# Performance work log

Hardware: AMD Instinct MI355X
Metric: run time of the kernel (lower is better)

Reference implementation:

```python
import jax, jax.numpy as jnp
import numpy as np

B, C, H, W, L = 8, 512, 32, 32, 10
CQK = C // 8
EPS = 1e-5


def conv1x1(x, Wt, b):
    # 1x1 conv == per-pixel linear: [O,C] x [B,C,H,W] -> [B,O,H,W]
    return jnp.einsum('oc,bchw->bohw', Wt, x) + b[None, :, None, None]


def batchnorm_train(x, g, b):
    # BatchNorm2d in training mode: batch stats over (N,H,W), biased variance
    m = x.mean(axis=(0, 2, 3))
    v = x.var(axis=(0, 2, 3))
    inv = jax.lax.rsqrt(v + EPS)
    return (x - m[None, :, None, None]) * (g * inv)[None, :, None, None] + b[None, :, None, None]


def setup_inputs() -> dict:
    key = jax.random.key(0)
    ks = jax.random.split(key, 24)
    s = lambda n: 1.0 / np.sqrt(n)
    inp = {
        'x': jax.random.normal(ks[0], (B, C, H, W), jnp.float32),
        'y': jax.random.normal(ks[1], (B, C, H, W), jnp.float32),
        'x_hidden': jax.random.normal(ks[2], (L, B, C, H, W), jnp.float32),
        'y_hidden': jax.random.normal(ks[3], (L, B, C, H, W), jnp.float32),
        'qW': jax.random.normal(ks[4], (CQK, C), jnp.float32) * s(C),
        'qb': jnp.zeros((CQK,), jnp.float32),
        'kW': jax.random.normal(ks[5], (CQK, C), jnp.float32) * s(C),
        'kb': jnp.zeros((CQK,), jnp.float32),
        'v1W': jax.random.normal(ks[6], (C, C), jnp.float32) * s(C),
        'v1b': jnp.zeros((C,), jnp.float32),
        'v2W': jax.random.normal(ks[7], (C, C), jnp.float32) * s(C),
        'v2b': jnp.zeros((C,), jnp.float32),
        'hw1': jnp.ones((L,), jnp.float32),
        'hw2': jnp.ones((L,), jnp.float32),
        'g1W1': jax.random.normal(ks[8], (64, C), jnp.float32) * s(C),
        'g1b1': jnp.zeros((64,), jnp.float32),
        'g1W2': jax.random.normal(ks[9], (1, 64), jnp.float32) * s(64),
        'g1b2': jnp.zeros((1,), jnp.float32),
        'g2W1': jax.random.normal(ks[10], (64, C), jnp.float32) * s(C),
        'g2b1': jnp.zeros((64,), jnp.float32),
        'g2W2': jax.random.normal(ks[11], (1, 64), jnp.float32) * s(64),
        'g2b2': jnp.zeros((1,), jnp.float32),
        'rW1': jax.random.normal(ks[12], (C, C), jnp.float32) * s(C),
        'rb1': jnp.zeros((C,), jnp.float32),
        'bn1g': jnp.ones((C,), jnp.float32),
        'bn1b': jnp.zeros((C,), jnp.float32),
        'rW2': jax.random.normal(ks[13], (C, C), jnp.float32) * s(C),
        'rb2': jnp.zeros((C,), jnp.float32),
        'bn2g': jnp.ones((C,), jnp.float32),
        'bn2b': jnp.zeros((C,), jnp.float32),
    }
    return inp


def reference(x, y, x_hidden, y_hidden, qW, qb, kW, kb, v1W, v1b, v2W, v2b,
              hw1, hw2, g1W1, g1b1, g1W2, g1b2, g2W1, g2b1, g2W2, g2b2,
              rW1, rb1, bn1g, bn1b, rW2, rb2, bn2g, bn2b):
    b_, c_, h_, w_ = x.shape
    n = h_ * w_

    def residual(z):
        z1 = jax.nn.relu(batchnorm_train(conv1x1(z, rW1, rb1), bn1g, bn1b))
        return batchnorm_train(conv1x1(z1, rW2, rb2), bn2g, bn2b)

    # QKV projections (1x1 convs), flattened to tokens
    q = conv1x1(x, qW, qb).reshape(b_, CQK, n).transpose(0, 2, 1)   # [B,N,Cqk]
    k = conv1x1(y, kW, kb).reshape(b_, CQK, n)                       # [B,Cqk,N]
    v1 = conv1x1(x, v1W, v1b).reshape(b_, c_, n)                     # [B,C,N]
    v2 = conv1x1(y, v2W, v2b).reshape(b_, c_, n)

    attn = jax.nn.softmax(jnp.einsum('bnd,bdm->bnm', q, k), axis=-1)  # [B,N,N]
    out1 = jnp.einsum('bcn,bmn->bcm', v1, attn).reshape(b_, c_, h_, w_)  # v1 @ attn^T
    out2 = jnp.einsum('bcn,bnm->bcm', v2, attn).reshape(b_, c_, h_, w_)  # v2 @ attn

    # hidden-layer weighted channel means -> gamma scalars
    num_layers = min(x_hidden.shape[0], L)
    xw = jax.nn.softmax(hw1[:num_layers])
    yw = jax.nn.softmax(hw2[:num_layers])
    x_hw = jnp.einsum('l,lbc->bc', xw, x_hidden[:num_layers].mean(axis=(3, 4)))  # [B,C]
    y_hw = jnp.einsum('l,lbc->bc', yw, y_hidden[:num_layers].mean(axis=(3, 4)))

    def gamma_gen(v, W1, b1, W2, b2):
        h1 = jax.nn.relu(v @ W1.T + b1)
        return (h1 @ W2.T + b2).reshape(b_, 1, 1, 1)

    gamma1 = gamma_gen(x_hw, g1W1, g1b1, g1W2, g1b2)
    gamma2 = gamma_gen(y_hw, g2W1, g2b1, g2W2, g2b2)

    out1 = jax.nn.relu(residual(gamma1 * out1) + x)
    out2 = jax.nn.relu(residual(gamma2 * out2) + y)
    return out1, out2
```

## Files before the change

kernel.cpp:

```cpp
#include <hip/hip_runtime.h>

#define BB 8
#define CC 512
#define NT 1024
#define LL 10
#define DQK 64
#define BN_EPS 1e-5f

using u16 = unsigned short;
typedef __attribute__((ext_vector_type(8))) short short8;
typedef __attribute__((ext_vector_type(4))) float f32x4;

__device__ __forceinline__ float waveSum(float v) {
#pragma unroll
  for (int o = 32; o; o >>= 1) v += __shfl_down(v, o, 64);
  return v;
}
__device__ __forceinline__ float waveMax(float v) {
#pragma unroll
  for (int o = 32; o; o >>= 1) v = fmaxf(v, __shfl_down(v, o, 64));
  return v;
}
__device__ __forceinline__ u16 f2bf(float f) {
  unsigned u = __float_as_uint(f);
  u += 0x7FFFu + ((u >> 16) & 1u);
  return (u16)(u >> 16);
}
__device__ __forceinline__ float bf2f(u16 h) {
  return __uint_as_float(((unsigned)h) << 16);
}
__device__ __forceinline__ void g2l16(const u16* g, void* l) {
  __builtin_amdgcn_global_load_lds(
      (const __attribute__((address_space(1))) unsigned int*)g,
      (__attribute__((address_space(3))) unsigned int*)l, 16, 0, 0);
}

__global__ __launch_bounds__(256) void hidden_mean_kernel(
    const float* __restrict__ xh, const float* __restrict__ yh, float* __restrict__ lm) {
  const int LBC = LL * BB * CC;
  int wid = blockIdx.x * 4 + (threadIdx.x >> 6);
  int lane = threadIdx.x & 63;
  int row0 = wid * 4;
  const float* src = xh;
  int r0 = row0;
  if (row0 >= LBC) { src = yh; r0 = row0 - LBC; }
  const float4* p = (const float4*)(src + (size_t)r0 * NT);
  float s[4];
#pragma unroll
  for (int r = 0; r < 4; r++) {
    float4 a = p[r * 256 + lane];
    float4 b = p[r * 256 + 64 + lane];
    float4 c = p[r * 256 + 128 + lane];
    float4 d = p[r * 256 + 192 + lane];
    s[r] = ((a.x + a.y) + (a.z + a.w)) + ((b.x + b.y) + (b.z + b.w)) +
           ((c.x + c.y) + (c.z + c.w)) + ((d.x + d.y) + (d.z + d.w));
  }
#pragma unroll
  for (int r = 0; r < 4; r++) s[r] = waveSum(s[r]);
  if (lane == 0) {
    float4 o = {s[0] * (1.0f / NT), s[1] * (1.0f / NT),
                s[2] * (1.0f / NT), s[3] * (1.0f / NT)};
    *(float4*)&lm[row0] = o;
  }
}

__global__ __launch_bounds__(256) void gamma_kernel(
    const float* __restrict__ lm,
    const float* __restrict__ hw1, const float* __restrict__ hw2,
    const float* __restrict__ g1W1, const float* __restrict__ g1b1,
    const float* __restrict__ g1W2, const float* __restrict__ g1b2,
    const float* __restrict__ g2W1, const float* __restrict__ g2b1,
    const float* __restrict__ g2W2, const float* __restrict__ g2b2,
    float* __restrict__ gamma) {
  int which = blockIdx.x >> 3;
  int b = blockIdx.x & 7;
  const float* hw = which ? hw2 : hw1;
  const float* W1 = which ? g2W1 : g1W1;
  const float* b1 = which ? g2b1 : g1b1;
  const float* W2 = which ? g2W2 : g1W2;
  const float* b2 = which ? g2b2 : g1b2;
  __shared__ float sxhw[CC];
  __shared__ float wsm[LL];
  if (threadIdx.x == 0) {
    float mx = -1e30f;
    for (int l = 0; l < LL; l++) mx = fmaxf(mx, hw[l]);
    float den = 0.f, e[LL];
    for (int l = 0; l < LL; l++) { e[l] = __expf(hw[l] - mx); den += e[l]; }
    for (int l = 0; l < LL; l++) wsm[l] = e[l] / den;
  }
  __syncthreads();
  const float* lmb = lm + (size_t)which * LL * BB * CC + b * CC;
  for (int c = threadIdx.x; c < CC; c += blockDim.x) {
    float a = 0.f;
    for (int l = 0; l < LL; l++) a += wsm[l] * lmb[l * BB * CC + c];
    sxhw[c] = a;
  }
  __syncthreads();
  float contrib = 0.f;
  if (threadIdx.x < 64) {
    int d = threadIdx.x;
    float a = b1[d];
    const float* wr = W1 + d * CC;
    for (int c = 0; c < CC; c++) a = fmaf(wr[c], sxhw[c], a);
    contrib = W2[d] * fmaxf(a, 0.f);
  }
  contrib = waveSum(contrib);
  if (threadIdx.x == 0) gamma[which * BB + b] = contrib + b2[0];
}

struct WcvtArgs {
  const float* src[4];
  int nblk[5];
};
__global__ __launch_bounds__(256) void wcvt_kernel(WcvtArgs a, u16* __restrict__ dst) {
  int blk = blockIdx.x;
  int seg = 0;
  while (blk >= a.nblk[seg + 1]) seg++;
  int rel = blk - a.nblk[seg];
  const float4* s4 = (const float4*)a.src[seg];
  float4 v = s4[(size_t)rel * 256 + threadIdx.x];
  uint2 o;
  o.x = (unsigned)f2bf(v.x) | ((unsigned)f2bf(v.y) << 16);
  o.y = (unsigned)f2bf(v.z) | ((unsigned)f2bf(v.w) << 16);
  ((uint2*)dst)[(size_t)blk * 256 + threadIdx.x] = o;
}

__global__ __launch_bounds__(256) void wcvt_split_kernel(
    const float* __restrict__ qW, const float* __restrict__ kW,
    u16* __restrict__ qh, u16* __restrict__ ql,
    u16* __restrict__ kh, u16* __restrict__ kl,
    const float* __restrict__ qb, const float* __restrict__ kb,
    const float* __restrict__ v1b, const float* __restrict__ v2b,
    float* __restrict__ qkb, float* __restrict__ vb) {
  int blk = blockIdx.x;
  if (blk == 0) {
    int t = threadIdx.x;
    if (t < 64) qkb[t] = qb[t];
    else if (t < 128) qkb[t] = kb[t - 64];
    vb[t] = v1b[t]; vb[t + 256] = v1b[t + 256];
    vb[t + 512] = v2b[t]; vb[t + 768] = v2b[t + 256];
  }
  const float* src = (blk < 32) ? qW : kW;
  u16* dh = (blk < 32) ? qh : kh;
  u16* dl = (blk < 32) ? ql : kl;
  int rel = blk & 31;
  float4 v = ((const float4*)src)[(size_t)rel * 256 + threadIdx.x];
  u16 h0 = f2bf(v.x), h1 = f2bf(v.y), h2 = f2bf(v.z), h3 = f2bf(v.w);
  u16 l0 = f2bf(v.x - bf2f(h0)), l1 = f2bf(v.y - bf2f(h1));
  u16 l2 = f2bf(v.z - bf2f(h2)), l3 = f2bf(v.w - bf2f(h3));
  uint2 oh, ol;
  oh.x = (unsigned)h0 | ((unsigned)h1 << 16); oh.y = (unsigned)h2 | ((unsigned)h3 << 16);
  ol.x = (unsigned)l0 | ((unsigned)l1 << 16); ol.y = (unsigned)l2 | ((unsigned)l3 << 16);
  ((uint2*)dh)[(size_t)rel * 256 + threadIdx.x] = oh;
  ((uint2*)dl)[(size_t)rel * 256 + threadIdx.x] = ol;
}

__global__ __launch_bounds__(256) void transpose_xy_kernel(
    const float* __restrict__ x, const float* __restrict__ y,
    u16* __restrict__ xth, u16* __restrict__ xtl,
    u16* __restrict__ yth, u16* __restrict__ ytl) {
  __shared__ float t[64][65];
  int z = blockIdx.z;
  const float* src = (z < 8) ? x : y;
  u16* dh = (z < 8) ? xth : yth;
  u16* dl = (z < 8) ? xtl : ytl;
  int b = z & 7;
  int n0 = blockIdx.x * 64, c0 = blockIdx.y * 64;
  int tc = threadIdx.x & 63, tr = threadIdx.x >> 6;
  const float* S = src + ((size_t)b * CC + c0) * NT + n0;
#pragma unroll
  for (int r = 0; r < 16; r++) {
    int c = tr + r * 4;
    t[c][tc] = S[(size_t)c * NT + tc];
  }
  __syncthreads();
  size_t base = ((size_t)b * NT + n0) * CC + c0;
#pragma unroll
  for (int r = 0; r < 16; r++) {
    int n = tr + r * 4;
    float v = t[tc][n];
    u16 h = f2bf(v);
    dh[base + (size_t)n * CC + tc] = h;
    dl[base + (size_t)n * CC + tc] = f2bf(v - bf2f(h));
  }
}

__global__ __launch_bounds__(256) void transpose_attn_kernel(
    const u16* __restrict__ attn, u16* __restrict__ attnT) {
  __shared__ u16 t[64][66];
  int b = blockIdx.z;
  int n0 = blockIdx.y * 64, m0 = blockIdx.x * 64;
  int tc = threadIdx.x & 63, tr = threadIdx.x >> 6;
  const u16* S = attn + ((size_t)b * NT + n0) * NT + m0;
#pragma unroll
  for (int r = 0; r < 16; r++) {
    int nr = tr + r * 4;
    t[nr][tc] = S[(size_t)nr * NT + tc];
  }
  __syncthreads();
  u16* D = attnT + ((size_t)b * NT + m0) * NT + n0;
#pragma unroll
  for (int r = 0; r < 16; r++) {
    int mr = tr + r * 4;
    D[(size_t)mr * NT + tc] = t[tc][mr];
  }
}

template <int BN>
__global__ __launch_bounds__(256) void gemm_bf16(
    const u16* __restrict__ A, long long sA, int lda,
    const u16* __restrict__ B, long long sB, long long sB2, int ldb,
    void* __restrict__ C, long long sC, int ldc,
    int K, int storef32,
    const float* __restrict__ bias_row, int brs,
    const float* __restrict__ scale) {
  constexpr int BM = 128, BK = 32;
  constexpr int WN = (BN == 128) ? 2 : 1;
  constexpr int WM = 4 / WN;
  constexpr int FM = BM / (WM * 16);
  constexpr int FN = BN / (WN * 16);
  __shared__ u16 As[BM * BK];
  __shared__ u16 Bs[BN * BK];
  const int bz = blockIdx.z;
  const int i0 = blockIdx.y * BM;
  const int j0 = blockIdx.x * BN;
  const u16* Ab = A + (size_t)bz * sA + (size_t)i0 * lda;
  const u16* Bb = B + (size_t)(bz & 7) * sB + (size_t)(bz >> 3) * sB2 + (size_t)j0 * ldb;
  const int tid = threadIdx.x;
  const int lane = tid & 63;
  const int wave = tid >> 6;
  const int wr = wave / WN, wc = wave % WN;
  const int fr = lane & 15;
  const int kg = lane >> 4;
  const int arow = tid >> 2;
  const int aq = tid & 3;

  f32x4 acc[FM][FN] = {};

  for (int k0 = 0; k0 < K; k0 += BK) {
#pragma unroll
    for (int c = 0; c < (BM * BK * 2) / 4096; c++)
      g2l16(Ab + (size_t)(arow + c * 64) * lda + k0 + aq * 8,
            (char*)As + c * 4096 + tid * 16);
#pragma unroll
    for (int c = 0; c < (BN * BK * 2) / 4096; c++)
      g2l16(Bb + (size_t)(arow + c * 64) * ldb + k0 + aq * 8,
            (char*)Bs + c * 4096 + tid * 16);
    __syncthreads();
    short8 fa[FM], fb[FN];
#pragma unroll
    for (int i = 0; i < FM; i++)
      fa[i] = *(const short8*)&As[(wr * FM * 16 + i * 16 + fr) * BK + kg * 8];
#pragma unroll
    for (int j = 0; j < FN; j++)
      fb[j] = *(const short8*)&Bs[(wc * FN * 16 + j * 16 + fr) * BK + kg * 8];
#pragma unroll
    for (int i = 0; i < FM; i++)
#pragma unroll
      for (int j = 0; j < FN; j++)
        acc[i][j] = __builtin_amdgcn_mfma_f32_16x16x32_bf16(fa[i], fb[j], acc[i][j], 0, 0, 0);
    __syncthreads();
  }

  const float scl = scale ? scale[bz] : 1.0f;
  const float* brow = bias_row ? bias_row + (size_t)bz * brs : nullptr;
  float* Cf = (float*)C + (size_t)bz * sC;
  u16* Ch = (u16*)C + (size_t)bz * sC;
#pragma unroll
  for (int i = 0; i < FM; i++) {
#pragma unroll
    for (int j = 0; j < FN; j++) {
      int col = j0 + wc * FN * 16 + j * 16 + fr;
#pragma unroll
      for (int r = 0; r < 4; r++) {
        int row = i0 + wr * FM * 16 + i * 16 + kg * 4 + r;
        float rb = brow ? brow[row] : 0.0f;
        float v = (acc[i][j][r] + rb) * scl;
        if (storef32) Cf[(size_t)row * ldc + col] = v;
        else Ch[(size_t)row * ldc + col] = f2bf(v);
      }
    }
  }
}

__global__ __launch_bounds__(256) void gemm_split(
    const u16* __restrict__ Ah_, const u16* __restrict__ Al_, long long sA, int lda,
    const u16* __restrict__ Bh_, const u16* __restrict__ Bl_, long long sB, int ldb,
    float* __restrict__ Cf, u16* __restrict__ Ch, u16* __restrict__ Cl,
    long long sC, int ldc, int K, const float* __restrict__ bias_col, int bcs) {
  constexpr int BM = 128, BN = 64, BK = 32;
  constexpr int FM = 2, FN = 4;
  __shared__ u16 Ahs[BM * BK];
  __shared__ u16 Als[BM * BK];
  __shared__ u16 Bhs[BN * BK];
  __shared__ u16 Bls[BN * BK];
  const int bz = blockIdx.z;
  const int i0 = blockIdx.y * BM;
  const int j0 = blockIdx.x * BN;
  const u16* Abh = Ah_ + (size_t)bz * sA + (size_t)i0 * lda;
  const u16* Abl = Al_ + (size_t)bz * sA + (size_t)i0 * lda;
  const u16* Bbh = Bh_ + (size_t)bz * sB + (size_t)j0 * ldb;
  const u16* Bbl = Bl_ + (size_t)bz * sB + (size_t)j0 * ldb;
  const int tid = threadIdx.x;
  const int lane = tid & 63;
  const int wr = tid >> 6;
  const int fr = lane & 15;
  const int kg = lane >> 4;
  const int arow = tid >> 2;
  const int aq = tid & 3;

  f32x4 acc[FM][FN] = {};

  for (int k0 = 0; k0 < K; k0 += BK) {
#pragma unroll
    for (int c = 0; c < 2; c++) {
      g2l16(Abh + (size_t)(arow + c * 64) * lda + k0 + aq * 8,
            (char*)Ahs + c * 4096 + tid * 16);
      g2l16(Abl + (size_t)(arow + c * 64) * lda + k0 + aq * 8,
            (char*)Als + c * 4096 + tid * 16);
    }
    g2l16(Bbh + (size_t)arow * ldb + k0 + aq * 8, (char*)Bhs + tid * 16);
    g2l16(Bbl + (size_t)arow * ldb + k0 + aq * 8, (char*)Bls + tid * 16);
    __syncthreads();
    short8 fah[FM], fal[FM], fbh[FN], fbl[FN];
#pragma unroll
    for (int i = 0; i < FM; i++) {
      fah[i] = *(const short8*)&Ahs[(wr * 32 + i * 16 + fr) * BK + kg * 8];
      fal[i] = *(const short8*)&Als[(wr * 32 + i * 16 + fr) * BK + kg * 8];
    }
#pragma unroll
    for (int j = 0; j < FN; j++) {
      fbh[j] = *(const short8*)&Bhs[(j * 16 + fr) * BK + kg * 8];
      fbl[j] = *(const short8*)&Bls[(j * 16 + fr) * BK + kg * 8];
    }
#pragma unroll
    for (int i = 0; i < FM; i++)
#pragma unroll
      for (int j = 0; j < FN; j++) {
        acc[i][j] = __builtin_amdgcn_mfma_f32_16x16x32_bf16(fah[i], fbh[j], acc[i][j], 0, 0, 0);
        acc[i][j] = __builtin_amdgcn_mfma_f32_16x16x32_bf16(fah[i], fbl[j], acc[i][j], 0, 0, 0);
        acc[i][j] = __builtin_amdgcn_mfma_f32_16x16x32_bf16(fal[i], fbh[j], acc[i][j], 0, 0, 0);
      }
    __syncthreads();
  }

  const float* bcol = bias_col ? bias_col + (size_t)bz * bcs : nullptr;
  float* Cfb = Cf ? Cf + (size_t)bz * sC : nullptr;
  u16* Chb = Ch ? Ch + (size_t)bz * sC : nullptr;
  u16* Clb = Cl ? Cl + (size_t)bz * sC : nullptr;
#pragma unroll
  for (int i = 0; i < FM; i++) {
#pragma unroll
    for (int j = 0; j < FN; j++) {
      int col = j0 + j * 16 + fr;
      float cb = bcol ? bcol[col] : 0.0f;
#pragma unroll
      for (int r = 0; r < 4; r++) {
        int row = i0 + wr * 32 + i * 16 + kg * 4 + r;
        float v = acc[i][j][r] + cb;
        if (Cfb) {
          Cfb[(size_t)row * ldc + col] = v;
        } else {
          u16 h = f2bf(v);
          Chb[(size_t)row * ldc + col] = h;
          Clb[(size_t)row * ldc + col] = f2bf(v - bf2f(h));
        }
      }
    }
  }
}

__global__ __launch_bounds__(256) void softmax_bf_kernel(
    const float* __restrict__ S, u16* __restrict__ A) {
  const float4* row = (const float4*)(S + (size_t)blockIdx.x * NT);
  float4 v = row[threadIdx.x];
  __shared__ float sb[4];
  __shared__ float broad;
  int lane = threadIdx.x & 63, wid = threadIdx.x >> 6;
  float mx = fmaxf(fmaxf(v.x, v.y), fmaxf(v.z, v.w));
  mx = waveMax(mx);
  if (lane == 0) sb[wid] = mx;
  __syncthreads();
  if (threadIdx.x == 0) broad = fmaxf(fmaxf(sb[0], sb[1]), fmaxf(sb[2], sb[3]));
  __syncthreads();
  mx = broad;
  v.x = __expf(v.x - mx); v.y = __expf(v.y - mx);
  v.z = __expf(v.z - mx); v.w = __expf(v.w - mx);
  float s = v.x + v.y + v.z + v.w;
  s = waveSum(s);
  __syncthreads();
  if (lane == 0) sb[wid] = s;
  __syncthreads();
  if (threadIdx.x == 0) broad = sb[0] + sb[1] + sb[2] + sb[3];
  __syncthreads();
  float inv = 1.0f / broad;
  uint2 o;
  o.x = (unsigned)f2bf(v.x * inv) | ((unsigned)f2bf(v.y * inv) << 16);
  o.y = (unsigned)f2bf(v.z * inv) | ((unsigned)f2bf(v.w * inv) << 16);
  ((uint2*)(A + (size_t)blockIdx.x * NT))[threadIdx.x] = o;
}

__global__ __launch_bounds__(256) void bnstats_tm_part(
    const u16* __restrict__ Z, float* __restrict__ pS, float* __restrict__ pS2) {
  int blk = blockIdx.x;
  int chain = blk >> 8, bl = blk & 255;
  int c2 = threadIdx.x;
  float s0 = 0, s1 = 0, q0 = 0, q1 = 0;
  const u16* base = Z + (size_t)blk * 32 * CC;
#pragma unroll 4
  for (int r = 0; r < 32; r++) {
    unsigned u = *(const unsigned*)(base + (size_t)r * CC + c2 * 2);
    float a = bf2f((u16)u), b = bf2f((u16)(u >> 16));
    s0 += a; q0 += a * a; s1 += b; q1 += b * b;
  }
  size_t co = (size_t)chain * 512;
  pS[(co + c2 * 2) * 256 + bl] = s0;
  pS[(co + c2 * 2 + 1) * 256 + bl] = s1;
  pS2[(co + c2 * 2) * 256 + bl] = q0;
  pS2[(co + c2 * 2 + 1) * 256 + bl] = q1;
}
__global__ __launch_bounds__(256) void bnstats_tm_reduce(
    const float* __restrict__ pS, const float* __restrict__ pS2,
    const float* __restrict__ g, const float* __restrict__ bet,
    float* __restrict__ scale, float* __restrict__ shift) {
  int cg = blockIdx.x;
  int c = cg & 511;
  float s = pS[(size_t)cg * 256 + threadIdx.x];
  float s2 = pS2[(size_t)cg * 256 + threadIdx.x];
  s = waveSum(s); s2 = waveSum(s2);
  __shared__ float sb[8];
  int lane = threadIdx.x & 63, wid = threadIdx.x >> 6;
  if (lane == 0) { sb[wid] = s; sb[wid + 4] = s2; }
  __syncthreads();
  if (threadIdx.x == 0) {
    float S = sb[0] + sb[1] + sb[2] + sb[3];
    float S2 = sb[4] + sb[5] + sb[6] + sb[7];
    const float invn = 1.0f / (BB * NT);
    float mean = S * invn;
    float var = S2 * invn - mean * mean;
    float inv = rsqrtf(var + BN_EPS);
    float sc = g[c] * inv;
    scale[cg] = sc;
    shift[cg] = bet[c] - mean * sc;
  }
}

__global__ __launch_bounds__(256) void bnstats_cm(
    const u16* __restrict__ Z, const float* __restrict__ g, const float* __restrict__ bet,
    float* __restrict__ scale, float* __restrict__ shift) {
  int cg = blockIdx.x;
  int c = cg & 511;
  const uint2* row = (const uint2*)(Z + (size_t)cg * (BB * NT));
  float s = 0, s2 = 0;
#pragma unroll
  for (int it = 0; it < 8; it++) {
    uint2 u = row[threadIdx.x + it * 256];
    float a = bf2f((u16)u.x), b = bf2f((u16)(u.x >> 16));
    float d = bf2f((u16)u.y), e = bf2f((u16)(u.y >> 16));
    s += a + b + d + e;
    s2 += a * a + b * b + d * d + e * e;
  }
  s = waveSum(s); s2 = waveSum(s2);
  __shared__ float sb[8];
  int lane = threadIdx.x & 63, wid = threadIdx.x >> 6;
  if (lane == 0) { sb[wid] = s; sb[wid + 4] = s2; }
  __syncthreads();
  if (threadIdx.x == 0) {
    float S = sb[0] + sb[1] + sb[2] + sb[3];
    float S2 = sb[4] + sb[5] + sb[6] + sb[7];
    const float invn = 1.0f / (BB * NT);
    float mean = S * invn;
    float var = S2 * invn - mean * mean;
    float inv = rsqrtf(var + BN_EPS);
    float sc = g[c] * inv;
    scale[cg] = sc;
    shift[cg] = bet[c] - mean * sc;
  }
}

__global__ __launch_bounds__(256) void bn_apply_kernel(
    const u16* __restrict__ Z, u16* __restrict__ Zo,
    const float* __restrict__ scale, const float* __restrict__ shift) {
  size_t e4 = (size_t)blockIdx.x * 256 + threadIdx.x;
  int chain = (int)(e4 >> 20);
  int c = (int)(e4 & 127) * 4 + chain * 512;
  uint2 u = ((const uint2*)Z)[e4];
  float a = bf2f((u16)u.x), b = bf2f((u16)(u.x >> 16));
  float d = bf2f((u16)u.y), e = bf2f((u16)(u.y >> 16));
  a = fmaxf(fmaf(a, scale[c], shift[c]), 0.f);
  b = fmaxf(fmaf(b, scale[c + 1], shift[c + 1]), 0.f);
  d = fmaxf(fmaf(d, scale[c + 2], shift[c + 2]), 0.f);
  e = fmaxf(fmaf(e, scale[c + 3], shift[c + 3]), 0.f);
  uint2 o;
  o.x = (unsigned)f2bf(a) | ((unsigned)f2bf(b) << 16);
  o.y = (unsigned)f2bf(d) | ((unsigned)f2bf(e) << 16);
  ((uint2*)Zo)[e4] = o;
}

__global__ __launch_bounds__(256) void bn_final_kernel(
    const u16* __restrict__ Z2, const float* __restrict__ X, const float* __restrict__ Y,
    const float* __restrict__ scale, const float* __restrict__ shift,
    float* __restrict__ Out) {
  size_t e = (size_t)blockIdx.x * 256 + threadIdx.x;
  int chain = (int)(e >> 20);
  size_t ec = e & 1048575;
  int c = (int)(ec >> 11);
  int r = (int)(ec & 2047);
  int b = r >> 8;
  uint2 u = ((const uint2*)Z2)[e];
  float a0 = bf2f((u16)u.x), a1 = bf2f((u16)(u.x >> 16));
  float a2 = bf2f((u16)u.y), a3 = bf2f((u16)(u.y >> 16));
  float sc = scale[c + chain * 512], sh = shift[c + chain * 512];
  size_t xi = ((size_t)b * CC + c) * 256 + (r & 255);
  const float* Xs = chain ? Y : X;
  float4 xv = ((const float4*)Xs)[xi];
  float4 o;
  o.x = fmaxf(fmaf(a0, sc, sh) + xv.x, 0.f);
  o.y = fmaxf(fmaf(a1, sc, sh) + xv.y, 0.f);
  o.z = fmaxf(fmaf(a2, sc, sh) + xv.z, 0.f);
  o.w = fmaxf(fmaf(a3, sc, sh) + xv.w, 0.f);
  ((float4*)(Out + (size_t)chain * 4194304))[xi] = o;
}

extern "C" void kernel_launch(void* const* d_in, const int* in_sizes, int n_in,
                              void* d_out, int out_size, void* d_ws, size_t ws_size,
                              hipStream_t stream) {
  (void)in_sizes; (void)n_in; (void)out_size; (void)ws_size;
  const float* x    = (const float*)d_in[0];
  const float* y    = (const float*)d_in[1];
  const float* xh   = (const float*)d_in[2];
  const float* yh   = (const float*)d_in[3];
  const float* qW   = (const float*)d_in[4];
  const float* qb   = (const float*)d_in[5];
  const float* kW   = (const float*)d_in[6];
  const float* kb   = (const float*)d_in[7];
  const float* v1W  = (const float*)d_in[8];
  const float* v1b  = (const float*)d_in[9];
  const float* v2W  = (const float*)d_in[10];
  const float* v2b  = (const float*)d_in[11];
  const float* hw1  = (const float*)d_in[12];
  const float* hw2  = (const float*)d_in[13];
  const float* g1W1 = (const float*)d_in[14];
  const float* g1b1 = (const float*)d_in[15];
  const float* g1W2 = (const float*)d_in[16];
  const float* g1b2 = (const float*)d_in[17];
  const float* g2W1 = (const float*)d_in[18];
  const float* g2b1 = (const float*)d_in[19];
  const float* g2W2 = (const float*)d_in[20];
  const float* g2b2 = (const float*)d_in[21];
  const float* rW1  = (const float*)d_in[22];
  const float* bn1g = (const float*)d_in[24];
  const float* bn1b = (const float*)d_in[25];
  const float* rW2  = (const float*)d_in[26];
  const float* bn2g = (const float*)d_in[28];
  const float* bn2b = (const float*)d_in[29];
  float* out = (float*)d_out;

  float* ws  = (float*)d_ws;
  float* lm  = ws;
  float* gam = ws + 81920;
  float* scA = ws + 81936;
  float* shA = ws + 82960;
  float* qkb = ws + 83984;
  float* vb  = ws + 84112;
  float* pS  = ws + 85136;
  float* pS2 = ws + 347280;
  float* S   = ws + 609424;
  u16* U     = (u16*)(ws + 8998032);
  u16* Wqh = U;
  u16* Wql = U + 32768;
  u16* Wkh = U + 65536;
  u16* Wkl = U + 98304;
  u16* Wv1 = U + 131072;
  u16* Wv2 = U + 393216;
  u16* Wr1 = U + 655360;
  u16* Wr2 = U + 917504;
  u16* xth = U + 1179648;
  u16* yth = xth + 4194304;
  u16* xtl = yth + 4194304;
  u16* ytl = xtl + 4194304;
  u16* q_h = ytl + 4194304;
  u16* q_l = q_h + 524288;
  u16* k_h = q_l + 524288;
  u16* k_l = k_h + 524288;
  u16* v1  = k_l + 524288;
  u16* v2  = v1 + 4194304;
  u16* attn  = v2 + 4194304;
  u16* attnT = attn + 8388608;
  u16* o1t = xth;
  u16* z0  = v1;
  u16* z1  = xth;
  u16* z2  = attn;

  WcvtArgs wa;
  wa.src[0] = v1W; wa.src[1] = v2W; wa.src[2] = rW1; wa.src[3] = rW2;
  int pref[5] = {0, 256, 512, 768, 1024};
  for (int i = 0; i < 5; i++) wa.nblk[i] = pref[i];
  wcvt_kernel<<<1024, 256, 0, stream>>>(wa, Wv1);
  wcvt_split_kernel<<<64, 256, 0, stream>>>(qW, kW, Wqh, Wql, Wkh, Wkl,
                                            qb, kb, v1b, v2b, qkb, vb);
  hidden_mean_kernel<<<5120, 256, 0, stream>>>(xh, yh, lm);
  gamma_kernel<<<16, 256, 0, stream>>>(lm, hw1, hw2, g1W1, g1b1, g1W2, g1b2,
                                       g2W1, g2b1, g2W2, g2b2, gam);

  transpose_xy_kernel<<<dim3(16, 8, 16), 256, 0, stream>>>(x, y, xth, xtl, yth, ytl);

  gemm_bf16<128><<<dim3(64, 4, 2), 256, 0, stream>>>(
      Wv1, 262144, CC, xth, 4194304, 0, CC, v1, 4194304, BB * NT, CC, 0, vb, 512, nullptr);
  gemm_split<<<dim3(1, 64, 2), 256, 0, stream>>>(
      xth, xtl, 4194304, CC, Wqh, Wql, 65536, CC,
      nullptr, q_h, q_l, 1048576, DQK, CC, qkb, 64);

  gemm_split<<<dim3(16, 8, 8), 256, 0, stream>>>(
      q_h, q_l, (long long)NT * DQK, DQK, k_h, k_l, (long long)NT * DQK, DQK,
      S, nullptr, nullptr, (long long)NT * NT, NT, DQK, nullptr, 0);
  softmax_bf_kernel<<<BB * NT, 256, 0, stream>>>(S, attn);
  transpose_attn_kernel<<<dim3(16, 16, 8), 256, 0, stream>>>(attn, attnT);

  gemm_bf16<128><<<dim3(4, 8, 16), 256, 0, stream>>>(
      attn, (long long)NT * NT, NT, v1, NT, 4194304, BB * NT,
      o1t, (long long)NT * CC, CC, NT, 0, nullptr, 0, gam);

  gemm_bf16<128><<<dim3(4, 64, 2), 256, 0, stream>>>(
      o1t, 4194304, CC, Wr1, 0, 0, CC, z0, 4194304, CC, CC, 0, nullptr, 0, nullptr);
  bnstats_tm_part<<<512, 256, 0, stream>>>(z0, pS, pS2);
  bnstats_tm_reduce<<<1024, 256, 0, stream>>>(pS, pS2, bn1g, bn1b, scA, shA);
  bn_apply_kernel<<<8192, 256, 0, stream>>>(z0, z1, scA, shA);
  gemm_bf16<128><<<dim3(64, 4, 2), 256, 0, stream>>>(
      Wr2, 0, CC, z1, 4194304, 0, CC, z2, 4194304, BB * NT, CC, 0, nullptr, 0, nullptr);
  bnstats_cm<<<1024, 256, 0, stream>>>(z2, bn2g, bn2b, scA, shA);
  bn_final_kernel<<<8192, 256, 0, stream>>>(z2, x, y, scA, shA, out);
}
```

Before: 320.1 us.

## Merge preprocessing kernels into one launch with nontemporal hidden-state loads

Four preprocessing kernels (hidden-layer means, bf16 weight conversion, hi/lo split of the q/k weights, and the x/y transpose-split) become one block-indexed kernel. The hidden-mean part now gives each wave one row instead of four and reads the large hidden tensors with nontemporal loads. The aim is to cut launch gaps, let the independent work overlap, and keep the streamed hidden data from polluting cache. In exchange, every block now reserves the transpose's shared-memory tile, which may reduce occupancy for the memory-bound mean blocks.

```diff
diff --git a/kernel.cpp b/kernel.cpp
--- a/kernel.cpp
+++ b/kernel.cpp
@@ -10,6 +10,7 @@
 using u16 = unsigned short;
 typedef __attribute__((ext_vector_type(8))) short short8;
 typedef __attribute__((ext_vector_type(4))) float f32x4;
+typedef __attribute__((ext_vector_type(4))) float nf4;
 
 __device__ __forceinline__ float waveSum(float v) {
 #pragma unroll
@@ -35,32 +36,94 @@
       (__attribute__((address_space(3))) unsigned int*)l, 16, 0, 0);
 }
 
-__global__ __launch_bounds__(256) void hidden_mean_kernel(
-    const float* __restrict__ xh, const float* __restrict__ yh, float* __restrict__ lm) {
-  const int LBC = LL * BB * CC;
-  int wid = blockIdx.x * 4 + (threadIdx.x >> 6);
-  int lane = threadIdx.x & 63;
-  int row0 = wid * 4;
-  const float* src = xh;
-  int r0 = row0;
-  if (row0 >= LBC) { src = yh; r0 = row0 - LBC; }
-  const float4* p = (const float4*)(src + (size_t)r0 * NT);
-  float s[4];
-#pragma unroll
-  for (int r = 0; r < 4; r++) {
-    float4 a = p[r * 256 + lane];
-    float4 b = p[r * 256 + 64 + lane];
-    float4 c = p[r * 256 + 128 + lane];
-    float4 d = p[r * 256 + 192 + lane];
-    s[r] = ((a.x + a.y) + (a.z + a.w)) + ((b.x + b.y) + (b.z + b.w)) +
-           ((c.x + c.y) + (c.z + c.w)) + ((d.x + d.y) + (d.z + d.w));
-  }
-#pragma unroll
-  for (int r = 0; r < 4; r++) s[r] = waveSum(s[r]);
-  if (lane == 0) {
-    float4 o = {s[0] * (1.0f / NT), s[1] * (1.0f / NT),
-                s[2] * (1.0f / NT), s[3] * (1.0f / NT)};
-    *(float4*)&lm[row0] = o;
+struct PreArgs {
+  const float *xh, *yh;
+  float* lm;
+  const float *v1W, *v2W, *rW1, *rW2;
+  u16* Wdst;
+  const float *qW, *kW;
+  u16 *qh, *ql, *kh, *kl;
+  const float *qb, *kb, *v1b, *v2b;
+  float *qkb, *vb;
+  const float *x, *y;
+  u16 *xth, *xtl, *yth, *ytl;
+};
+__global__ __launch_bounds__(256) void pre_kernel(PreArgs a) {
+  __shared__ float t[64][65];
+  const int blk = blockIdx.x;
+  if (blk < 20480) {
+    int wid = blk * 4 + (threadIdx.x >> 6);
+    int lane = threadIdx.x & 63;
+    const int LBC = LL * BB * CC;
+    const float* src = a.xh;
+    int r = wid;
+    if (wid >= LBC) { src = a.yh; r = wid - LBC; }
+    const nf4* p = (const nf4*)(src + (size_t)r * NT);
+    nf4 v0 = __builtin_nontemporal_load(p + lane);
+    nf4 v1 = __builtin_nontemporal_load(p + 64 + lane);
+    nf4 v2 = __builtin_nontemporal_load(p + 128 + lane);
+    nf4 v3 = __builtin_nontemporal_load(p + 192 + lane);
+    float s = ((v0.x + v0.y) + (v0.z + v0.w)) + ((v1.x + v1.y) + (v1.z + v1.w)) +
+              ((v2.x + v2.y) + (v2.z + v2.w)) + ((v3.x + v3.y) + (v3.z + v3.w));
+    s = waveSum(s);
+    if (lane == 0) a.lm[wid] = s * (1.0f / NT);
+  } else if (blk < 21504) {
+    int rel = blk - 20480;
+    const float* srcs[4] = {a.v1W, a.v2W, a.rW1, a.rW2};
+    const float4* s4 = (const float4*)srcs[rel >> 8];
+    int r = rel & 255;
+    float4 v = s4[(size_t)r * 256 + threadIdx.x];
+    uint2 o;
+    o.x = (unsigned)f2bf(v.x) | ((unsigned)f2bf(v.y) << 16);
+    o.y = (unsigned)f2bf(v.z) | ((unsigned)f2bf(v.w) << 16);
+    ((uint2*)a.Wdst)[(size_t)rel * 256 + threadIdx.x] = o;
+  } else if (blk < 21568) {
+    int rel = blk - 21504;
+    if (rel == 0) {
+      int tt = threadIdx.x;
+      if (tt < 64) a.qkb[tt] = a.qb[tt];
+      else if (tt < 128) a.qkb[tt] = a.kb[tt - 64];
+      a.vb[tt] = a.v1b[tt]; a.vb[tt + 256] = a.v1b[tt + 256];
+      a.vb[tt + 512] = a.v2b[tt]; a.vb[tt + 768] = a.v2b[tt + 256];
+    }
+    const float* src = (rel < 32) ? a.qW : a.kW;
+    u16* dh = (rel < 32) ? a.qh : a.kh;
+    u16* dl = (rel < 32) ? a.ql : a.kl;
+    int r = rel & 31;
+    float4 v = ((const float4*)src)[(size_t)r * 256 + threadIdx.x];
+    u16 h0 = f2bf(v.x), h1 = f2bf(v.y), h2 = f2bf(v.z), h3 = f2bf(v.w);
+    u16 l0 = f2bf(v.x - bf2f(h0)), l1 = f2bf(v.y - bf2f(h1));
+    u16 l2 = f2bf(v.z - bf2f(h2)), l3 = f2bf(v.w - bf2f(h3));
+    uint2 oh, ol;
+    oh.x = (unsigned)h0 | ((unsigned)h1 << 16); oh.y = (unsigned)h2 | ((unsigned)h3 << 16);
+    ol.x = (unsigned)l0 | ((unsigned)l1 << 16); ol.y = (unsigned)l2 | ((unsigned)l3 << 16);
+    ((uint2*)dh)[(size_t)r * 256 + threadIdx.x] = oh;
+    ((uint2*)dl)[(size_t)r * 256 + threadIdx.x] = ol;
+  } else {
+    int rel = blk - 21568;
+    int z = rel >> 7;
+    const float* src = (z < 8) ? a.x : a.y;
+    u16* dh = (z < 8) ? a.xth : a.yth;
+    u16* dl = (z < 8) ? a.xtl : a.ytl;
+    int b = z & 7;
+    int n0 = (rel & 15) * 64, c0 = ((rel >> 4) & 7) * 64;
+    int tc = threadIdx.x & 63, tr = threadIdx.x >> 6;
+    const float* S = src + ((size_t)b * CC + c0) * NT + n0;
+#pragma unroll
+    for (int r = 0; r < 16; r++) {
+      int c = tr + r * 4;
+      t[c][tc] = S[(size_t)c * NT + tc];
+    }
+    __syncthreads();
+    size_t base = ((size_t)b * NT + n0) * CC + c0;
+#pragma unroll
+    for (int r = 0; r < 16; r++) {
+      int n = tr + r * 4;
+      float v = t[tc][n];
+      u16 h = f2bf(v);
+      dh[base + (size_t)n * CC + tc] = h;
+      dl[base + (size_t)n * CC + tc] = f2bf(v - bf2f(h));
+    }
   }
 }
 
@@ -106,83 +169,6 @@
   }
   contrib = waveSum(contrib);
   if (threadIdx.x == 0) gamma[which * BB + b] = contrib + b2[0];
-}
-
-struct WcvtArgs {
-  const float* src[4];
-  int nblk[5];
-};
-__global__ __launch_bounds__(256) void wcvt_kernel(WcvtArgs a, u16* __restrict__ dst) {
-  int blk = blockIdx.x;
-  int seg = 0;
-  while (blk >= a.nblk[seg + 1]) seg++;
-  int rel = blk - a.nblk[seg];
-  const float4* s4 = (const float4*)a.src[seg];
-  float4 v = s4[(size_t)rel * 256 + threadIdx.x];
-  uint2 o;
-  o.x = (unsigned)f2bf(v.x) | ((unsigned)f2bf(v.y) << 16);
-  o.y = (unsigned)f2bf(v.z) | ((unsigned)f2bf(v.w) << 16);
-  ((uint2*)dst)[(size_t)blk * 256 + threadIdx.x] = o;
-}
-
-__global__ __launch_bounds__(256) void wcvt_split_kernel(
-    const float* __restrict__ qW, const float* __restrict__ kW,
-    u16* __restrict__ qh, u16* __restrict__ ql,
-    u16* __restrict__ kh, u16* __restrict__ kl,
-    const float* __restrict__ qb, const float* __restrict__ kb,
-    const float* __restrict__ v1b, const float* __restrict__ v2b,
-    float* __restrict__ qkb, float* __restrict__ vb) {
-  int blk = blockIdx.x;
-  if (blk == 0) {
-    int t = threadIdx.x;
-    if (t < 64) qkb[t] = qb[t];
-    else if (t < 128) qkb[t] = kb[t - 64];
-    vb[t] = v1b[t]; vb[t + 256] = v1b[t + 256];
-    vb[t + 512] = v2b[t]; vb[t + 768] = v2b[t + 256];
-  }
-  const float* src = (blk < 32) ? qW : kW;
-  u16* dh = (blk < 32) ? qh : kh;
-  u16* dl = (blk < 32) ? ql : kl;
-  int rel = blk & 31;
-  float4 v = ((const float4*)src)[(size_t)rel * 256 + threadIdx.x];
-  u16 h0 = f2bf(v.x), h1 = f2bf(v.y), h2 = f2bf(v.z), h3 = f2bf(v.w);
-  u16 l0 = f2bf(v.x - bf2f(h0)), l1 = f2bf(v.y - bf2f(h1));
-  u16 l2 = f2bf(v.z - bf2f(h2)), l3 = f2bf(v.w - bf2f(h3));
-  uint2 oh, ol;
-  oh.x = (unsigned)h0 | ((unsigned)h1 << 16); oh.y = (unsigned)h2 | ((unsigned)h3 << 16);
-  ol.x = (unsigned)l0 | ((unsigned)l1 << 16); ol.y = (unsigned)l2 | ((unsigned)l3 << 16);
-  ((uint2*)dh)[(size_t)rel * 256 + threadIdx.x] = oh;
-  ((uint2*)dl)[(size_t)rel * 256 + threadIdx.x] = ol;
-}
-
-__global__ __launch_bounds__(256) void transpose_xy_kernel(
-    const float* __restrict__ x, const float* __restrict__ y,
-    u16* __restrict__ xth, u16* __restrict__ xtl,
-    u16* __restrict__ yth, u16* __restrict__ ytl) {
-  __shared__ float t[64][65];
-  int z = blockIdx.z;
-  const float* src = (z < 8) ? x : y;
-  u16* dh = (z < 8) ? xth : yth;
-  u16* dl = (z < 8) ? xtl : ytl;
-  int b = z & 7;
-  int n0 = blockIdx.x * 64, c0 = blockIdx.y * 64;
-  int tc = threadIdx.x & 63, tr = threadIdx.x >> 6;
-  const float* S = src + ((size_t)b * CC + c0) * NT + n0;
-#pragma unroll
-  for (int r = 0; r < 16; r++) {
-    int c = tr + r * 4;
-    t[c][tc] = S[(size_t)c * NT + tc];
-  }
-  __syncthreads();
-  size_t base = ((size_t)b * NT + n0) * CC + c0;
-#pragma unroll
-  for (int r = 0; r < 16; r++) {
-    int n = tr + r * 4;
-    float v = t[tc][n];
-    u16 h = f2bf(v);
-    dh[base + (size_t)n * CC + tc] = h;
-    dl[base + (size_t)n * CC + tc] = f2bf(v - bf2f(h));
-  }
 }
 
 __global__ __launch_bounds__(256) void transpose_attn_kernel(
@@ -592,18 +578,15 @@
   u16* z1  = xth;
   u16* z2  = attn;
 
-  WcvtArgs wa;
-  wa.src[0] = v1W; wa.src[1] = v2W; wa.src[2] = rW1; wa.src[3] = rW2;
-  int pref[5] = {0, 256, 512, 768, 1024};
-  for (int i = 0; i < 5; i++) wa.nblk[i] = pref[i];
-  wcvt_kernel<<<1024, 256, 0, stream>>>(wa, Wv1);
-  wcvt_split_kernel<<<64, 256, 0, stream>>>(qW, kW, Wqh, Wql, Wkh, Wkl,
-                                            qb, kb, v1b, v2b, qkb, vb);
-  hidden_mean_kernel<<<5120, 256, 0, stream>>>(xh, yh, lm);
+  PreArgs pa;
+  pa.xh = xh; pa.yh = yh; pa.lm = lm;
+  pa.v1W = v1W; pa.v2W = v2W; pa.rW1 = rW1; pa.rW2 = rW2; pa.Wdst = Wv1;
+  pa.qW = qW; pa.kW = kW; pa.qh = Wqh; pa.ql = Wql; pa.kh = Wkh; pa.kl = Wkl;
+  pa.qb = qb; pa.kb = kb; pa.v1b = v1b; pa.v2b = v2b; pa.qkb = qkb; pa.vb = vb;
+  pa.x = x; pa.y = y; pa.xth = xth; pa.xtl = xtl; pa.yth = yth; pa.ytl = ytl;
+  pre_kernel<<<23616, 256, 0, stream>>>(pa);
   gamma_kernel<<<16, 256, 0, stream>>>(lm, hw1, hw2, g1W1, g1b1, g1W2, g1b2,
                                        g2W1, g2b1, g2W2, g2b2, gam);
-
-  transpose_xy_kernel<<<dim3(16, 8, 16), 256, 0, stream>>>(x, y, xth, xtl, yth, ytl);
 
   gemm_bf16<128><<<dim3(64, 4, 2), 256, 0, stream>>>(
       Wv1, 262144, CC, xth, 4194304, 0, CC, v1, 4194304, BB * NT, CC, 0, vb, 512, nullptr);
```

Measured after the change: 275.4 us. -13.9%, faster.
